# Performance work log

Measured on AMD Instinct MI355X. Metric: run time of the kernel, lower is better.

## Reference

```python
import jax, jax.numpy as jnp
import numpy as np

N_NODES = 100000
N_EDGES = 3200000
N_FEAT = 128
HIDDEN = 16
N_CLASSES = 10
N_GRAPHS = 512


def setup_inputs() -> dict:
    key = jax.random.key(0)
    ks = jax.random.split(key, 12)
    x = jax.random.normal(ks[0], (N_NODES, N_FEAT), dtype=jnp.float32)
    edge_index = jax.random.randint(ks[1], (2, N_EDGES), 0, N_NODES, dtype=jnp.int64)
    batch = jnp.sort(jax.random.randint(ks[2], (N_NODES,), 0, N_GRAPHS, dtype=jnp.int64))
    def glorot(k, fan_in, fan_out):
        s = jnp.sqrt(6.0 / (fan_in + fan_out)).astype(jnp.float32)
        return jax.random.uniform(k, (fan_in, fan_out), jnp.float32, -s, s)
    W1 = glorot(ks[3], N_FEAT, HIDDEN); b1 = jnp.zeros((HIDDEN,), jnp.float32)
    W2 = glorot(ks[4], HIDDEN, HIDDEN); b2 = jnp.zeros((HIDDEN,), jnp.float32)
    W3 = glorot(ks[5], HIDDEN, HIDDEN); b3 = jnp.zeros((HIDDEN,), jnp.float32)
    Wlin = glorot(ks[6], HIDDEN, N_CLASSES)
    blin = jnp.zeros((N_CLASSES,), jnp.float32)
    return {"x": x, "edge_index": edge_index, "batch": batch,
            "W1": W1, "b1": b1, "W2": W2, "b2": b2, "W3": W3, "b3": b3,
            "Wlin": Wlin, "blin": blin}


def _gcn_conv(x, W, b, src, dst, norm, n):
    # h = X W ; out[dst] += norm * h[src] ; + bias
    h = x @ W
    out = jax.ops.segment_sum(h[src] * norm[:, None], dst, num_segments=n)
    return out + b


def reference(x, edge_index, batch, W1, b1, W2, b2, W3, b3, Wlin, blin):
    n = x.shape[0]
    loop = jnp.arange(n, dtype=edge_index.dtype)
    src = jnp.concatenate([edge_index[0], loop])  # add self-loops (PyG GCNConv default)
    dst = jnp.concatenate([edge_index[1], loop])
    # symmetric degree normalization: deg over destination (incl. self-loops)
    deg = jax.ops.segment_sum(jnp.ones_like(dst, dtype=x.dtype), dst, num_segments=n)
    dinv = jnp.where(deg > 0, jax.lax.rsqrt(jnp.maximum(deg, 1.0)), 0.0)
    norm = dinv[src] * dinv[dst]  # [E+N]

    h = jax.nn.relu(_gcn_conv(x, W1, b1, src, dst, norm, n))
    h = jax.nn.relu(_gcn_conv(h, W2, b2, src, dst, norm, n))
    h = _gcn_conv(h, W3, b3, src, dst, norm, n)
    # global add pool over graphs
    pooled = jax.ops.segment_sum(h, batch, num_segments=N_GRAPHS)  # [G, hidden]
    # dropout p=0.5 is identity in eval mode
    return pooled @ Wlin + blin
```

## Files before the change

### kernel.cpp

```cpp
#include <hip/hip_runtime.h>
#include <hip/hip_fp16.h>

#define N_NODES   100000
#define N_EDGES   3200000
#define N_FEAT    128
#define HIDDEN    16
#define N_CLASSES 10
#define N_GRAPHS  512
#define NPB       256
#define NBUCKET   391
#define EPB       4096
#define PBLK      ((N_EDGES + EPB - 1) / EPB)
#define PSLACK    15872
#define CSLACK    11520


__global__ void init_kernel(int* __restrict__ cur, __half* __restrict__ gA, __half* __restrict__ gB) {
    int i = blockIdx.x * 256 + threadIdx.x;
    if (i < NBUCKET) cur[i] = i * PSLACK;
    if (blockIdx.x == 0) {
        int tid = threadIdx.x;
        const __half2 z2 = __floats2half2_rn(0.f, 0.f);
        if (tid < 8)       ((__half2*)(gA + (size_t)N_NODES * HIDDEN))[tid] = z2;
        else if (tid < 16) ((__half2*)(gB + (size_t)N_NODES * HIDDEN))[tid - 8] = z2;
    }
}


__global__ __launch_bounds__(512) void partition_kernel(const int* __restrict__ src,
                                                        const int* __restrict__ dst,
                                                        int* __restrict__ cur,
                                                        unsigned* __restrict__ part) {
    __shared__ int cnt[NBUCKET];
    __shared__ int lbase[NBUCKET];
    __shared__ int rk[NBUCKET];
    __shared__ int gbase[NBUCKET];
    __shared__ int s[512];
    __shared__ unsigned sorted[EPB];
    __shared__ unsigned short bb[EPB];
    __shared__ unsigned char  dl[EPB];
    int tid = threadIdx.x;
    for (int i = tid; i < NBUCKET; i += 512) cnt[i] = 0;
    __syncthreads();
    int s0 = blockIdx.x * EPB;
#pragma unroll
    for (int i = 0; i < EPB / 512; ++i) {
        int le = i * 512 + tid;
        int e  = s0 + le;
        if (e < N_EDGES) {
            int d = dst[e];
            int b = d >> 8;
            bb[le] = (unsigned short)b;
            dl[le] = (unsigned char)(d & 255);
            atomicAdd(&cnt[b], 1);
        }
    }
    __syncthreads();
    int v = (tid < NBUCKET) ? cnt[tid] : 0;
    s[tid] = v;
    __syncthreads();
    for (int off = 1; off < 512; off <<= 1) {
        int t = (tid >= off) ? s[tid - off] : 0;
        __syncthreads();
        s[tid] += t;
        __syncthreads();
    }
    if (tid < NBUCKET) {
        int lb = s[tid] - v;
        lbase[tid] = lb;
        rk[tid]    = lb;
        int cpad = (v + 15) & ~15;
        gbase[tid] = cpad ? atomicAdd(&cur[tid], cpad) : 0;
    }
    __syncthreads();
#pragma unroll
    for (int i = 0; i < EPB / 512; ++i) {
        int le = i * 512 + tid;
        int e  = s0 + le;
        if (e < N_EDGES) {
            int b = bb[le];
            int r = atomicAdd(&rk[b], 1);
            sorted[r] = (unsigned)src[e] | ((unsigned)dl[le] << 17);
        }
    }
    __syncthreads();
    int w16 = tid >> 4, l16 = tid & 15;
    for (int b = w16; b < NBUCKET; b += 32) {
        int c = cnt[b];
        if (!c) continue;
        int cpad = (c + 15) & ~15;
        int lb = lbase[b], gb = gbase[b];
        for (int j = l16; j < cpad; j += 16)
            part[gb + j] = (j < c) ? sorted[lb + j] : 0xFFFFFFFFu;
    }
}

__global__ __launch_bounds__(512) void build_csr_kernel(const unsigned* __restrict__ part,
                                                        const int* __restrict__ cur,
                                                        int2* __restrict__ rp,
                                                        float* __restrict__ dinv, int* __restrict__ csr) {
    __shared__ int ncnt[256];
    __shared__ int s[512];
    int b   = blockIdx.x;
    int tid = threadIdx.x;
    int beg = b * PSLACK, end = cur[b];
    if (tid < 256) ncnt[tid] = 0;
    __syncthreads();
    for (int j = beg + tid; j < end; j += 512) {
        unsigned r = part[j];
        if (r != 0xFFFFFFFFu) atomicAdd(&ncnt[(r >> 17) & 255], 1);
    }
    __syncthreads();
    int deg = (tid < 256) ? ncnt[tid] : 0;
    int dp  = (deg + 15) & ~15;
    s[tid] = dp;
    __syncthreads();
    for (int off = 1; off < 512; off <<= 1) {
        int t = (tid >= off) ? s[tid - off] : 0;
        __syncthreads();
        s[tid] += t;
        __syncthreads();
    }
    int excl = s[tid] - dp;
    int cbeg = b * CSLACK;
    if (tid < 256) {
        int node = b * 256 + tid;
        if (node < N_NODES) {
            rp[node]   = make_int2(cbeg + excl, cbeg + excl + dp);
            dinv[node] = rsqrtf((float)(deg + 1));
            for (int p = deg; p < dp; ++p) csr[cbeg + excl + p] = N_NODES;
        }
    }
    __syncthreads();
    if (tid < 256) ncnt[tid] = cbeg + excl;
    __syncthreads();
    for (int j = beg + tid; j < end; j += 512) {
        unsigned r = part[j];
        if (r != 0xFFFFFFFFu) {
            int vv = (r >> 17) & 255;
            int slot = atomicAdd(&ncnt[vv], 1);
            csr[slot] = (int)(r & 0x1FFFFu);
        }
    }
}


__device__ __forceinline__ void pack_store8(__half* outp, int idx, const float* o) {
    int4 w;
    __half2 q;
    q = __floats2half2_rn(o[0], o[1]); w.x = *(int*)&q;
    q = __floats2half2_rn(o[2], o[3]); w.y = *(int*)&q;
    q = __floats2half2_rn(o[4], o[5]); w.z = *(int*)&q;
    q = __floats2half2_rn(o[6], o[7]); w.w = *(int*)&q;
    ((int4*)outp)[idx] = w;
}

__global__ __launch_bounds__(256) void transform_x_kernel(const float* __restrict__ x,
                                                          const float* __restrict__ W,
                                                          const float* __restrict__ dinv,
                                                          __half* __restrict__ g) {
    __shared__ __half2 Wp[1024];
    int tid = threadIdx.x;
    for (int i = tid; i < 1024; i += 256) {
        int kp = i >> 4, f = i & 15;
        Wp[i] = __floats2half2_rn(W[(2 * kp) * HIDDEN + f], W[(2 * kp + 1) * HIDDEN + f]);
    }
    __syncthreads();
    int l  = tid & 63;
    int wv = tid >> 6;
    int rw = l >> 2;
    int q  = l & 3;
    int row = blockIdx.x * 64 + wv * 16 + rw;
    if (row >= N_NODES) return;
    const float4* xp = (const float4*)x + (size_t)row * 32;
    float4 xr[8];
#pragma unroll
    for (int s8 = 0; s8 < 8; ++s8) xr[s8] = xp[q + 4 * s8];
    __half2 acc[16];
    const __half2 z2 = __floats2half2_rn(0.f, 0.f);
#pragma unroll
    for (int f = 0; f < 16; ++f) acc[f] = z2;
    const int4* w4 = (const int4*)Wp;
#pragma unroll
    for (int s8 = 0; s8 < 8; ++s8) {
        int k4 = q + 4 * s8;
        __half2 xp0 = __floats2half2_rn(xr[s8].x, xr[s8].y);
        __half2 xp1 = __floats2half2_rn(xr[s8].z, xr[s8].w);
#pragma unroll
        for (int hf = 0; hf < 2; ++hf) {
            int kp = 2 * k4 + hf;
            __half2 xv = hf ? xp1 : xp0;
#pragma unroll
            for (int j = 0; j < 4; ++j) {
                int4 wj = w4[kp * 4 + j];
                const __half2* wvv = (const __half2*)&wj;
#pragma unroll
                for (int ff = 0; ff < 4; ++ff)
                    acc[j * 4 + ff] = __hfma2(xv, wvv[ff], acc[j * 4 + ff]);
            }
        }
    }
    float di = dinv[row];
    float o[16];
#pragma unroll
    for (int f = 0; f < 16; ++f) {
        float2 t = __half22float2(acc[f]);
        float sv = t.x + t.y;
        sv += __shfl_xor(sv, 1);
        sv += __shfl_xor(sv, 2);
        o[f] = sv * di;
    }
    if (q == 0) {
        pack_store8(g, row * 2,     &o[0]);
        pack_store8(g, row * 2 + 1, &o[8]);
    }
}

template <int MODE>
__global__ __launch_bounds__(256) void aggregate_kernel(
        const __half* __restrict__ g, const int2* __restrict__ rp,
        const int* __restrict__ csr, const float* __restrict__ dinv,
        const float* __restrict__ bias, const float* __restrict__ Wn,
        __half* __restrict__ out) {
    __shared__ float WnL[HIDDEN * HIDDEN];
    int tid  = threadIdx.x;
    int wave = tid >> 6;
    int l    = tid & 63;
    int c  = l >> 3;
    int vl = (l >> 1) & 3;
    int hh = l & 1;
    int v = blockIdx.x * 16 + wave * 4 + vl;
    int2 range = rp[v];
    if (MODE == 2) {
        if (tid < HIDDEN * HIDDEN) WnL[tid] = Wn[tid];
        __syncthreads();
    }
    int b2 = range.x >> 1;
    int K  = (range.y - range.x) >> 4;
    const int2* csr2 = (const int2*)csr;
    const int4* g4 = (const int4*)g;
    float a0 = 0.f, a1 = 0.f, a2 = 0.f, a3 = 0.f, a4 = 0.f, a5 = 0.f, a6 = 0.f, a7 = 0.f;
    for (int i = 0; i < K; ++i) {
        int2 ss = csr2[b2 + c + 8 * i];
        int4 r0 = g4[ss.x * 2 + hh];
        int4 r1 = g4[ss.y * 2 + hh];
        float2 f0 = __half22float2(*(const __half2*)&r0.x);
        float2 f1 = __half22float2(*(const __half2*)&r0.y);
        float2 f2 = __half22float2(*(const __half2*)&r0.z);
        float2 f3 = __half22float2(*(const __half2*)&r0.w);
        a0 += f0.x; a1 += f0.y; a2 += f1.x; a3 += f1.y;
        a4 += f2.x; a5 += f2.y; a6 += f3.x; a7 += f3.y;
        float2 g0 = __half22float2(*(const __half2*)&r1.x);
        float2 g1 = __half22float2(*(const __half2*)&r1.y);
        float2 g2 = __half22float2(*(const __half2*)&r1.z);
        float2 g3 = __half22float2(*(const __half2*)&r1.w);
        a0 += g0.x; a1 += g0.y; a2 += g1.x; a3 += g1.y;
        a4 += g2.x; a5 += g2.y; a6 += g3.x; a7 += g3.y;
    }
    a0 += __shfl_xor(a0, 8);  a1 += __shfl_xor(a1, 8);
    a2 += __shfl_xor(a2, 8);  a3 += __shfl_xor(a3, 8);
    a4 += __shfl_xor(a4, 8);  a5 += __shfl_xor(a5, 8);
    a6 += __shfl_xor(a6, 8);  a7 += __shfl_xor(a7, 8);
    a0 += __shfl_xor(a0, 16); a1 += __shfl_xor(a1, 16);
    a2 += __shfl_xor(a2, 16); a3 += __shfl_xor(a3, 16);
    a4 += __shfl_xor(a4, 16); a5 += __shfl_xor(a5, 16);
    a6 += __shfl_xor(a6, 16); a7 += __shfl_xor(a7, 16);
    a0 += __shfl_xor(a0, 32); a1 += __shfl_xor(a1, 32);
    a2 += __shfl_xor(a2, 32); a3 += __shfl_xor(a3, 32);
    a4 += __shfl_xor(a4, 32); a5 += __shfl_xor(a5, 32);
    a6 += __shfl_xor(a6, 32); a7 += __shfl_xor(a7, 32);
    if (c == 0) {
        int4 r = g4[v * 2 + hh];
        float2 s0 = __half22float2(*(const __half2*)&r.x);
        float2 s1 = __half22float2(*(const __half2*)&r.y);
        float2 s2 = __half22float2(*(const __half2*)&r.z);
        float2 s3 = __half22float2(*(const __half2*)&r.w);
        float di = dinv[v];
        const float4* bp = (const float4*)bias;
        float4 bA = bp[hh * 2];
        float4 bB = bp[hh * 2 + 1];
        float o[8];
        o[0] = di * (a0 + s0.x) + bA.x;
        o[1] = di * (a1 + s0.y) + bA.y;
        o[2] = di * (a2 + s1.x) + bA.z;
        o[3] = di * (a3 + s1.y) + bA.w;
        o[4] = di * (a4 + s2.x) + bB.x;
        o[5] = di * (a5 + s2.y) + bB.y;
        o[6] = di * (a6 + s3.x) + bB.z;
        o[7] = di * (a7 + s3.y) + bB.w;
        if (MODE == 2) {
#pragma unroll
            for (int i = 0; i < 8; ++i) o[i] = fmaxf(o[i], 0.f);
            float pa[16];
#pragma unroll
            for (int f = 0; f < 16; ++f) pa[f] = 0.f;
            const float* wr = &WnL[hh * 8 * HIDDEN];
#pragma unroll
            for (int qq = 0; qq < 8; ++qq) {
                float hq = o[qq];
#pragma unroll
                for (int f = 0; f < 16; ++f) pa[f] += hq * wr[qq * HIDDEN + f];
            }
            float o2[8];
#pragma unroll
            for (int i = 0; i < 8; ++i) {
                float lo = pa[i];
                float hi = pa[8 + i];
                float keep = hh ? hi : lo;
                float send = hh ? lo : hi;
                float recv = __shfl_xor(send, 1);
                o2[i] = di * (keep + recv);
            }
            pack_store8(out, v * 2 + hh, o2);
        } else {
            pack_store8(out, v * 2 + hh, o);
        }
    }
}


__global__ void pool_head_kernel(const __half* __restrict__ h, const int* __restrict__ batch,
                                 const float* __restrict__ Wlin, const float* __restrict__ blin,
                                 float* __restrict__ out) {
    __shared__ float red[256];
    __shared__ int bounds[2];
    int g   = blockIdx.x;
    int tid = threadIdx.x;
    if (tid < 2) {
        int target = g + tid;
        int lo = 0, hi = N_NODES;
        while (lo < hi) {
            int mid = (lo + hi) >> 1;
            if (batch[mid] < target) lo = mid + 1; else hi = mid;
        }
        bounds[tid] = lo;
    }
    __syncthreads();
    int start = bounds[0], end = bounds[1];
    int f = tid & 15, r = tid >> 4;
    float acc = 0.f;
    for (int v = start + r; v < end; v += 16)
        acc += __half2float(h[v * HIDDEN + f]);
    red[tid] = acc;
    __syncthreads();
    for (int off = 128; off >= 16; off >>= 1) {
        if (tid < off) red[tid] += red[tid + off];
        __syncthreads();
    }
    if (tid < N_CLASSES) {
        float s = blin[tid];
#pragma unroll
        for (int fe = 0; fe < HIDDEN; ++fe) s += red[fe] * Wlin[fe * N_CLASSES + tid];
        out[g * N_CLASSES + tid] = s;
    }
}


extern "C" void kernel_launch(void* const* d_in, const int* in_sizes, int n_in,
                              void* d_out, int out_size, void* d_ws, size_t ws_size,
                              hipStream_t stream) {
    const float* x     = (const float*)d_in[0];
    const int*   ei    = (const int*)d_in[1];
    const int*   src   = ei;
    const int*   dst   = ei + N_EDGES;
    const int*   batch = (const int*)d_in[2];
    const float* W1 = (const float*)d_in[3];
    const float* b1 = (const float*)d_in[4];
    const float* W2 = (const float*)d_in[5];
    const float* b2 = (const float*)d_in[6];
    const float* W3 = (const float*)d_in[7];
    const float* b3 = (const float*)d_in[8];
    const float* Wlin = (const float*)d_in[9];
    const float* blin = (const float*)d_in[10];
    float* out = (float*)d_out;

    char* w = (char*)d_ws;
    auto alloc = [&](size_t bytes) -> char* {
        char* p = w;
        w += (bytes + 255) & ~(size_t)255;
        return p;
    };
    int*    cur    = (int*)alloc((size_t)NBUCKET * 4);
    int2*   rp     = (int2*)alloc((size_t)N_NODES * 8);
    float*  dinv   = (float*)alloc((size_t)N_NODES * 4);
    __half* gA     = (__half*)alloc((size_t)(N_NODES + 1) * HIDDEN * 2);
    __half* gB     = (__half*)alloc((size_t)(N_NODES + 1) * HIDDEN * 2);
    __half* hA     = (__half*)alloc((size_t)(N_NODES + 1) * HIDDEN * 2);
    unsigned* part = (unsigned*)alloc((size_t)NBUCKET * PSLACK * 4);
    int*    csr    = (int*)alloc((size_t)NBUCKET * CSLACK * 4);

    int ntx = (N_NODES + 63) / 64;
    int ab  = (N_NODES + 15) / 16;

    init_kernel<<<(NBUCKET + 255) / 256, 256, 0, stream>>>(cur, gA, gB);
    partition_kernel<<<PBLK, 512, 0, stream>>>(src, dst, cur, part);
    build_csr_kernel<<<NBUCKET, 512, 0, stream>>>(part, cur, rp, dinv, csr);

    transform_x_kernel<<<ntx, 256, 0, stream>>>(x, W1, dinv, gA);
    aggregate_kernel<2><<<ab, 256, 0, stream>>>(gA, rp, csr, dinv, b1, W2, gB);
    aggregate_kernel<2><<<ab, 256, 0, stream>>>(gB, rp, csr, dinv, b2, W3, gA);
    aggregate_kernel<0><<<ab, 256, 0, stream>>>(gA, rp, csr, dinv, b3, nullptr, hA);

    pool_head_kernel<<<N_GRAPHS, 256, 0, stream>>>(hA, batch, Wlin, blin, out);
}
```

Before: 266.9 us.

## Fuse GCN pipeline into one persistent kernel with grid barriers

Replaces the seven separate launches with one persistent 512-block kernel. Phases are separated by atomic grid-wide barriers: partition, work-stolen X·W1 transform, CSR build, three aggregations and pooling. The X·W1 transform is now computed before degrees are known, written as fp32 to a temporary buffer and scaled by dinv inside the CSR build, so it can overlap with partitioning. This is meant to remove launch gaps and tail idle time, but it relies on all 512 blocks being co-resident, and the partition step now runs 256 threads per block instead of 512.

```diff
diff --git a/kernel.cpp b/kernel.cpp
--- a/kernel.cpp
+++ b/kernel.cpp
@@ -7,141 +7,39 @@
 #define HIDDEN    16
 #define N_CLASSES 10
 #define N_GRAPHS  512
-#define NPB       256
 #define NBUCKET   391
 #define EPB       4096
-#define PBLK      ((N_EDGES + EPB - 1) / EPB)
+#define PBLK      782
 #define PSLACK    15872
 #define CSLACK    11520
-
-
-__global__ void init_kernel(int* __restrict__ cur, __half* __restrict__ gA, __half* __restrict__ gB) {
-    int i = blockIdx.x * 256 + threadIdx.x;
-    if (i < NBUCKET) cur[i] = i * PSLACK;
-    if (blockIdx.x == 0) {
-        int tid = threadIdx.x;
-        const __half2 z2 = __floats2half2_rn(0.f, 0.f);
-        if (tid < 8)       ((__half2*)(gA + (size_t)N_NODES * HIDDEN))[tid] = z2;
-        else if (tid < 16) ((__half2*)(gB + (size_t)N_NODES * HIDDEN))[tid - 8] = z2;
-    }
-}
-
-
-__global__ __launch_bounds__(512) void partition_kernel(const int* __restrict__ src,
-                                                        const int* __restrict__ dst,
-                                                        int* __restrict__ cur,
-                                                        unsigned* __restrict__ part) {
-    __shared__ int cnt[NBUCKET];
-    __shared__ int lbase[NBUCKET];
-    __shared__ int rk[NBUCKET];
-    __shared__ int gbase[NBUCKET];
-    __shared__ int s[512];
-    __shared__ unsigned sorted[EPB];
-    __shared__ unsigned short bb[EPB];
-    __shared__ unsigned char  dl[EPB];
-    int tid = threadIdx.x;
-    for (int i = tid; i < NBUCKET; i += 512) cnt[i] = 0;
-    __syncthreads();
-    int s0 = blockIdx.x * EPB;
-#pragma unroll
-    for (int i = 0; i < EPB / 512; ++i) {
-        int le = i * 512 + tid;
-        int e  = s0 + le;
-        if (e < N_EDGES) {
-            int d = dst[e];
-            int b = d >> 8;
-            bb[le] = (unsigned short)b;
-            dl[le] = (unsigned char)(d & 255);
-            atomicAdd(&cnt[b], 1);
-        }
-    }
-    __syncthreads();
-    int v = (tid < NBUCKET) ? cnt[tid] : 0;
-    s[tid] = v;
-    __syncthreads();
-    for (int off = 1; off < 512; off <<= 1) {
-        int t = (tid >= off) ? s[tid - off] : 0;
-        __syncthreads();
-        s[tid] += t;
-        __syncthreads();
-    }
-    if (tid < NBUCKET) {
-        int lb = s[tid] - v;
-        lbase[tid] = lb;
-        rk[tid]    = lb;
-        int cpad = (v + 15) & ~15;
-        gbase[tid] = cpad ? atomicAdd(&cur[tid], cpad) : 0;
-    }
-    __syncthreads();
-#pragma unroll
-    for (int i = 0; i < EPB / 512; ++i) {
-        int le = i * 512 + tid;
-        int e  = s0 + le;
-        if (e < N_EDGES) {
-            int b = bb[le];
-            int r = atomicAdd(&rk[b], 1);
-            sorted[r] = (unsigned)src[e] | ((unsigned)dl[le] << 17);
-        }
-    }
-    __syncthreads();
-    int w16 = tid >> 4, l16 = tid & 15;
-    for (int b = w16; b < NBUCKET; b += 32) {
-        int c = cnt[b];
-        if (!c) continue;
-        int cpad = (c + 15) & ~15;
-        int lb = lbase[b], gb = gbase[b];
-        for (int j = l16; j < cpad; j += 16)
-            part[gb + j] = (j < c) ? sorted[lb + j] : 0xFFFFFFFFu;
-    }
-}
-
-__global__ __launch_bounds__(512) void build_csr_kernel(const unsigned* __restrict__ part,
-                                                        const int* __restrict__ cur,
-                                                        int2* __restrict__ rp,
-                                                        float* __restrict__ dinv, int* __restrict__ csr) {
-    __shared__ int ncnt[256];
-    __shared__ int s[512];
-    int b   = blockIdx.x;
-    int tid = threadIdx.x;
-    int beg = b * PSLACK, end = cur[b];
-    if (tid < 256) ncnt[tid] = 0;
-    __syncthreads();
-    for (int j = beg + tid; j < end; j += 512) {
-        unsigned r = part[j];
-        if (r != 0xFFFFFFFFu) atomicAdd(&ncnt[(r >> 17) & 255], 1);
-    }
-    __syncthreads();
-    int deg = (tid < 256) ? ncnt[tid] : 0;
-    int dp  = (deg + 15) & ~15;
-    s[tid] = dp;
-    __syncthreads();
-    for (int off = 1; off < 512; off <<= 1) {
-        int t = (tid >= off) ? s[tid - off] : 0;
-        __syncthreads();
-        s[tid] += t;
-        __syncthreads();
-    }
-    int excl = s[tid] - dp;
-    int cbeg = b * CSLACK;
-    if (tid < 256) {
-        int node = b * 256 + tid;
-        if (node < N_NODES) {
-            rp[node]   = make_int2(cbeg + excl, cbeg + excl + dp);
-            dinv[node] = rsqrtf((float)(deg + 1));
-            for (int p = deg; p < dp; ++p) csr[cbeg + excl + p] = N_NODES;
-        }
-    }
-    __syncthreads();
-    if (tid < 256) ncnt[tid] = cbeg + excl;
-    __syncthreads();
-    for (int j = beg + tid; j < end; j += 512) {
-        unsigned r = part[j];
-        if (r != 0xFFFFFFFFu) {
-            int vv = (r >> 17) & 255;
-            int slot = atomicAdd(&ncnt[vv], 1);
-            csr[slot] = (int)(r & 0x1FFFFu);
-        }
-    }
+#define GRID      512
+#define BLK       256
+#define TX_UNITS  1563
+#define AGG_UNITS 6250
+
+
+struct PartLDS {
+    int cnt[NBUCKET]; int lbase[NBUCKET]; int rk[NBUCKET]; int gbase[NBUCKET];
+    int s[512];
+    unsigned sorted[EPB];
+    unsigned short bb[EPB];
+    unsigned char  dl[EPB];
+};
+struct CsrLDS  { int ncnt[256]; int s[256]; };
+struct TxLDS   { __half2 Wp[1024]; };
+struct AggLDS  { float WnL[256]; };
+struct PoolLDS { float red[256]; int bounds[2]; };
+union AllLDS { PartLDS p; CsrLDS c; TxLDS t; AggLDS a; PoolLDS o; };
+
+
+__device__ __forceinline__ void grid_sync(int* bar, int target) {
+    __syncthreads();
+    if (threadIdx.x == 0) {
+        __hip_atomic_fetch_add(bar, 1, __ATOMIC_ACQ_REL, __HIP_MEMORY_SCOPE_AGENT);
+        while (__hip_atomic_load(bar, __ATOMIC_ACQUIRE, __HIP_MEMORY_SCOPE_AGENT) < target)
+            __builtin_amdgcn_s_sleep(2);
+    }
+    __syncthreads();
 }
 
 
@@ -155,22 +53,131 @@
     ((int4*)outp)[idx] = w;
 }
 
-__global__ __launch_bounds__(256) void transform_x_kernel(const float* __restrict__ x,
-                                                          const float* __restrict__ W,
-                                                          const float* __restrict__ dinv,
-                                                          __half* __restrict__ g) {
-    __shared__ __half2 Wp[1024];
+
+__device__ void partition_block(int pb, const int* __restrict__ src, const int* __restrict__ dst,
+                                int* __restrict__ cur, unsigned* __restrict__ part, PartLDS& L) {
     int tid = threadIdx.x;
-    for (int i = tid; i < 1024; i += 256) {
-        int kp = i >> 4, f = i & 15;
-        Wp[i] = __floats2half2_rn(W[(2 * kp) * HIDDEN + f], W[(2 * kp + 1) * HIDDEN + f]);
-    }
-    __syncthreads();
+    for (int i = tid; i < NBUCKET; i += BLK) L.cnt[i] = 0;
+    __syncthreads();
+    int s0 = pb * EPB;
+#pragma unroll
+    for (int i = 0; i < EPB / BLK; ++i) {
+        int le = i * BLK + tid;
+        int e  = s0 + le;
+        if (e < N_EDGES) {
+            int d = dst[e];
+            int b = d >> 8;
+            L.bb[le] = (unsigned short)b;
+            L.dl[le] = (unsigned char)(d & 255);
+            atomicAdd(&L.cnt[b], 1);
+        }
+    }
+    __syncthreads();
+    int t2 = tid + 256;
+    int v0 = (tid < NBUCKET) ? L.cnt[tid] : 0;
+    int v1 = (t2  < NBUCKET) ? L.cnt[t2]  : 0;
+    L.s[tid] = v0; L.s[t2] = v1;
+    __syncthreads();
+    for (int off = 1; off < 512; off <<= 1) {
+        int a = (tid >= off) ? L.s[tid - off] : 0;
+        int b = (t2  >= off) ? L.s[t2  - off] : 0;
+        __syncthreads();
+        L.s[tid] += a; L.s[t2] += b;
+        __syncthreads();
+    }
+    if (tid < NBUCKET) {
+        int lb = L.s[tid] - v0;
+        L.lbase[tid] = lb; L.rk[tid] = lb;
+        int cpad = (v0 + 15) & ~15;
+        L.gbase[tid] = cpad ? atomicAdd(&cur[tid], cpad) : 0;
+    }
+    if (t2 < NBUCKET) {
+        int lb = L.s[t2] - v1;
+        L.lbase[t2] = lb; L.rk[t2] = lb;
+        int cpad = (v1 + 15) & ~15;
+        L.gbase[t2] = cpad ? atomicAdd(&cur[t2], cpad) : 0;
+    }
+    __syncthreads();
+#pragma unroll
+    for (int i = 0; i < EPB / BLK; ++i) {
+        int le = i * BLK + tid;
+        int e  = s0 + le;
+        if (e < N_EDGES) {
+            int b = L.bb[le];
+            int r = atomicAdd(&L.rk[b], 1);
+            L.sorted[r] = (unsigned)src[e] | ((unsigned)L.dl[le] << 17);
+        }
+    }
+    __syncthreads();
+    int w16 = tid >> 4, l16 = tid & 15;
+    for (int b = w16; b < NBUCKET; b += 16) {
+        int c = L.cnt[b];
+        if (!c) continue;
+        int cpad = (c + 15) & ~15;
+        int lb = L.lbase[b], gb = L.gbase[b];
+        for (int j = l16; j < cpad; j += 16)
+            part[gb + j] = (j < c) ? L.sorted[lb + j] : 0xFFFFFFFFu;
+    }
+}
+
+__device__ void csr_block(int b, const unsigned* __restrict__ part, const int* __restrict__ cur,
+                          int2* __restrict__ rp, float* __restrict__ dinv, int* __restrict__ csr,
+                          const float* __restrict__ xw, __half* __restrict__ gA, CsrLDS& L) {
+    int tid = threadIdx.x;
+    int beg = b * PSLACK, end = cur[b];
+    L.ncnt[tid] = 0;
+    __syncthreads();
+    for (int j = beg + tid; j < end; j += BLK) {
+        unsigned r = part[j];
+        if (r != 0xFFFFFFFFu) atomicAdd(&L.ncnt[(r >> 17) & 255], 1);
+    }
+    __syncthreads();
+    int deg = L.ncnt[tid];
+    int dp  = (deg + 15) & ~15;
+    L.s[tid] = dp;
+    __syncthreads();
+    for (int off = 1; off < 256; off <<= 1) {
+        int t = (tid >= off) ? L.s[tid - off] : 0;
+        __syncthreads();
+        L.s[tid] += t;
+        __syncthreads();
+    }
+    int excl = L.s[tid] - dp;
+    int cbeg = b * CSLACK;
+    int node = b * 256 + tid;
+    if (node < N_NODES) {
+        rp[node] = make_int2(cbeg + excl, cbeg + excl + dp);
+        float di = rsqrtf((float)(deg + 1));
+        dinv[node] = di;
+        for (int p = deg; p < dp; ++p) csr[cbeg + excl + p] = N_NODES;
+        const float4* ip = (const float4*)(xw + (size_t)node * 16);
+        float4 v0 = ip[0], v1 = ip[1], v2 = ip[2], v3 = ip[3];
+        float o0[8] = {v0.x*di, v0.y*di, v0.z*di, v0.w*di, v1.x*di, v1.y*di, v1.z*di, v1.w*di};
+        float o1[8] = {v2.x*di, v2.y*di, v2.z*di, v2.w*di, v3.x*di, v3.y*di, v3.z*di, v3.w*di};
+        pack_store8(gA, node * 2,     o0);
+        pack_store8(gA, node * 2 + 1, o1);
+    }
+    __syncthreads();
+    L.ncnt[tid] = cbeg + excl;
+    __syncthreads();
+    for (int j = beg + tid; j < end; j += BLK) {
+        unsigned r = part[j];
+        if (r != 0xFFFFFFFFu) {
+            int vv = (r >> 17) & 255;
+            int slot = atomicAdd(&L.ncnt[vv], 1);
+            csr[slot] = (int)(r & 0x1FFFFu);
+        }
+    }
+}
+
+__device__ __forceinline__ void tx_unit(int u, const float* __restrict__ x,
+                                        float* __restrict__ xw, const __half2* Wp) {
+    int tid = threadIdx.x;
     int l  = tid & 63;
     int wv = tid >> 6;
     int rw = l >> 2;
     int q  = l & 3;
-    int row = blockIdx.x * 64 + wv * 16 + rw;
+    int row = u * 64 + wv * 16 + rw;
     if (row >= N_NODES) return;
     const float4* xp = (const float4*)x + (size_t)row * 32;
     float4 xr[8];
@@ -200,7 +207,6 @@
             }
         }
     }
-    float di = dinv[row];
     float o[16];
 #pragma unroll
     for (int f = 0; f < 16; ++f) {
@@ -208,151 +214,214 @@
         float sv = t.x + t.y;
         sv += __shfl_xor(sv, 1);
         sv += __shfl_xor(sv, 2);
-        o[f] = sv * di;
+        o[f] = sv;
     }
     if (q == 0) {
-        pack_store8(g, row * 2,     &o[0]);
-        pack_store8(g, row * 2 + 1, &o[8]);
+        float4* op = (float4*)(xw + (size_t)row * 16);
+        op[0] = make_float4(o[0],  o[1],  o[2],  o[3]);
+        op[1] = make_float4(o[4],  o[5],  o[6],  o[7]);
+        op[2] = make_float4(o[8],  o[9],  o[10], o[11]);
+        op[3] = make_float4(o[12], o[13], o[14], o[15]);
     }
 }
 
 template <int MODE>
-__global__ __launch_bounds__(256) void aggregate_kernel(
-        const __half* __restrict__ g, const int2* __restrict__ rp,
-        const int* __restrict__ csr, const float* __restrict__ dinv,
-        const float* __restrict__ bias, const float* __restrict__ Wn,
-        __half* __restrict__ out) {
-    __shared__ float WnL[HIDDEN * HIDDEN];
-    int tid  = threadIdx.x;
+__device__ void agg_phase(const __half* __restrict__ g, const int2* __restrict__ rp,
+                          const int* __restrict__ csr, const float* __restrict__ dinv,
+                          const float* __restrict__ bias, const float* __restrict__ Wn,
+                          __half* __restrict__ out, AggLDS& L) {
+    int tid = threadIdx.x;
+    if (MODE == 2) L.WnL[tid] = Wn[tid];
+    __syncthreads();
     int wave = tid >> 6;
     int l    = tid & 63;
     int c  = l >> 3;
     int vl = (l >> 1) & 3;
     int hh = l & 1;
-    int v = blockIdx.x * 16 + wave * 4 + vl;
-    int2 range = rp[v];
-    if (MODE == 2) {
-        if (tid < HIDDEN * HIDDEN) WnL[tid] = Wn[tid];
-        __syncthreads();
-    }
-    int b2 = range.x >> 1;
-    int K  = (range.y - range.x) >> 4;
     const int2* csr2 = (const int2*)csr;
     const int4* g4 = (const int4*)g;
-    float a0 = 0.f, a1 = 0.f, a2 = 0.f, a3 = 0.f, a4 = 0.f, a5 = 0.f, a6 = 0.f, a7 = 0.f;
-    for (int i = 0; i < K; ++i) {
-        int2 ss = csr2[b2 + c + 8 * i];
-        int4 r0 = g4[ss.x * 2 + hh];
-        int4 r1 = g4[ss.y * 2 + hh];
-        float2 f0 = __half22float2(*(const __half2*)&r0.x);
-        float2 f1 = __half22float2(*(const __half2*)&r0.y);
-        float2 f2 = __half22float2(*(const __half2*)&r0.z);
-        float2 f3 = __half22float2(*(const __half2*)&r0.w);
-        a0 += f0.x; a1 += f0.y; a2 += f1.x; a3 += f1.y;
-        a4 += f2.x; a5 += f2.y; a6 += f3.x; a7 += f3.y;
-        float2 g0 = __half22float2(*(const __half2*)&r1.x);
-        float2 g1 = __half22float2(*(const __half2*)&r1.y);
-        float2 g2 = __half22float2(*(const __half2*)&r1.z);
-        float2 g3 = __half22float2(*(const __half2*)&r1.w);
-        a0 += g0.x; a1 += g0.y; a2 += g1.x; a3 += g1.y;
-        a4 += g2.x; a5 += g2.y; a6 += g3.x; a7 += g3.y;
-    }
-    a0 += __shfl_xor(a0, 8);  a1 += __shfl_xor(a1, 8);
-    a2 += __shfl_xor(a2, 8);  a3 += __shfl_xor(a3, 8);
-    a4 += __shfl_xor(a4, 8);  a5 += __shfl_xor(a5, 8);
-    a6 += __shfl_xor(a6, 8);  a7 += __shfl_xor(a7, 8);
-    a0 += __shfl_xor(a0, 16); a1 += __shfl_xor(a1, 16);
-    a2 += __shfl_xor(a2, 16); a3 += __shfl_xor(a3, 16);
-    a4 += __shfl_xor(a4, 16); a5 += __shfl_xor(a5, 16);
-    a6 += __shfl_xor(a6, 16); a7 += __shfl_xor(a7, 16);
-    a0 += __shfl_xor(a0, 32); a1 += __shfl_xor(a1, 32);
-    a2 += __shfl_xor(a2, 32); a3 += __shfl_xor(a3, 32);
-    a4 += __shfl_xor(a4, 32); a5 += __shfl_xor(a5, 32);
-    a6 += __shfl_xor(a6, 32); a7 += __shfl_xor(a7, 32);
-    if (c == 0) {
-        int4 r = g4[v * 2 + hh];
-        float2 s0 = __half22float2(*(const __half2*)&r.x);
-        float2 s1 = __half22float2(*(const __half2*)&r.y);
-        float2 s2 = __half22float2(*(const __half2*)&r.z);
-        float2 s3 = __half22float2(*(const __half2*)&r.w);
-        float di = dinv[v];
-        const float4* bp = (const float4*)bias;
-        float4 bA = bp[hh * 2];
-        float4 bB = bp[hh * 2 + 1];
-        float o[8];
-        o[0] = di * (a0 + s0.x) + bA.x;
-        o[1] = di * (a1 + s0.y) + bA.y;
-        o[2] = di * (a2 + s1.x) + bA.z;
-        o[3] = di * (a3 + s1.y) + bA.w;
-        o[4] = di * (a4 + s2.x) + bB.x;
-        o[5] = di * (a5 + s2.y) + bB.y;
-        o[6] = di * (a6 + s3.x) + bB.z;
-        o[7] = di * (a7 + s3.y) + bB.w;
-        if (MODE == 2) {
-#pragma unroll
-            for (int i = 0; i < 8; ++i) o[i] = fmaxf(o[i], 0.f);
-            float pa[16];
-#pragma unroll
-            for (int f = 0; f < 16; ++f) pa[f] = 0.f;
-            const float* wr = &WnL[hh * 8 * HIDDEN];
-#pragma unroll
-            for (int qq = 0; qq < 8; ++qq) {
-                float hq = o[qq];
-#pragma unroll
-                for (int f = 0; f < 16; ++f) pa[f] += hq * wr[qq * HIDDEN + f];
+    for (int unit = blockIdx.x; unit < AGG_UNITS; unit += GRID) {
+        int v = unit * 16 + wave * 4 + vl;
+        int2 range = rp[v];
+        int b2 = range.x >> 1;
+        int K  = (range.y - range.x) >> 4;
+        float a0 = 0.f, a1 = 0.f, a2 = 0.f, a3 = 0.f, a4 = 0.f, a5 = 0.f, a6 = 0.f, a7 = 0.f;
+        for (int i = 0; i < K; ++i) {
+            int2 ss = csr2[b2 + c + 8 * i];
+            int4 r0 = g4[ss.x * 2 + hh];
+            int4 r1 = g4[ss.y * 2 + hh];
+            float2 f0 = __half22float2(*(const __half2*)&r0.x);
+            float2 f1 = __half22float2(*(const __half2*)&r0.y);
+            float2 f2 = __half22float2(*(const __half2*)&r0.z);
+            float2 f3 = __half22float2(*(const __half2*)&r0.w);
+            a0 += f0.x; a1 += f0.y; a2 += f1.x; a3 += f1.y;
+            a4 += f2.x; a5 += f2.y; a6 += f3.x; a7 += f3.y;
+            float2 g0 = __half22float2(*(const __half2*)&r1.x);
+            float2 g1 = __half22float2(*(const __half2*)&r1.y);
+            float2 g2 = __half22float2(*(const __half2*)&r1.z);
+            float2 g3 = __half22float2(*(const __half2*)&r1.w);
+            a0 += g0.x; a1 += g0.y; a2 += g1.x; a3 += g1.y;
+            a4 += g2.x; a5 += g2.y; a6 += g3.x; a7 += g3.y;
+        }
+        a0 += __shfl_xor(a0, 8);  a1 += __shfl_xor(a1, 8);
+        a2 += __shfl_xor(a2, 8);  a3 += __shfl_xor(a3, 8);
+        a4 += __shfl_xor(a4, 8);  a5 += __shfl_xor(a5, 8);
+        a6 += __shfl_xor(a6, 8);  a7 += __shfl_xor(a7, 8);
+        a0 += __shfl_xor(a0, 16); a1 += __shfl_xor(a1, 16);
+        a2 += __shfl_xor(a2, 16); a3 += __shfl_xor(a3, 16);
+        a4 += __shfl_xor(a4, 16); a5 += __shfl_xor(a5, 16);
+        a6 += __shfl_xor(a6, 16); a7 += __shfl_xor(a7, 16);
+        a0 += __shfl_xor(a0, 32); a1 += __shfl_xor(a1, 32);
+        a2 += __shfl_xor(a2, 32); a3 += __shfl_xor(a3, 32);
+        a4 += __shfl_xor(a4, 32); a5 += __shfl_xor(a5, 32);
+        a6 += __shfl_xor(a6, 32); a7 += __shfl_xor(a7, 32);
+        if (c == 0) {
+            int4 r = g4[v * 2 + hh];
+            float2 s0 = __half22float2(*(const __half2*)&r.x);
+            float2 s1 = __half22float2(*(const __half2*)&r.y);
+            float2 s2 = __half22float2(*(const __half2*)&r.z);
+            float2 s3 = __half22float2(*(const __half2*)&r.w);
+            float di = dinv[v];
+            const float4* bp = (const float4*)bias;
+            float4 bA = bp[hh * 2];
+            float4 bB = bp[hh * 2 + 1];
+            float o[8];
+            o[0] = di * (a0 + s0.x) + bA.x;
+            o[1] = di * (a1 + s0.y) + bA.y;
+            o[2] = di * (a2 + s1.x) + bA.z;
+            o[3] = di * (a3 + s1.y) + bA.w;
+            o[4] = di * (a4 + s2.x) + bB.x;
+            o[5] = di * (a5 + s2.y) + bB.y;
+            o[6] = di * (a6 + s3.x) + bB.z;
+            o[7] = di * (a7 + s3.y) + bB.w;
+            if (MODE == 2) {
+#pragma unroll
+                for (int i = 0; i < 8; ++i) o[i] = fmaxf(o[i], 0.f);
+                float pa[16];
+#pragma unroll
+                for (int f = 0; f < 16; ++f) pa[f] = 0.f;
+                const float* wr = &L.WnL[hh * 8 * HIDDEN];
+#pragma unroll
+                for (int qq = 0; qq < 8; ++qq) {
+                    float hq = o[qq];
+#pragma unroll
+                    for (int f = 0; f < 16; ++f) pa[f] += hq * wr[qq * HIDDEN + f];
+                }
+                float o2[8];
+#pragma unroll
+                for (int i = 0; i < 8; ++i) {
+                    float lo = pa[i];
+                    float hi = pa[8 + i];
+                    float keep = hh ? hi : lo;
+                    float send = hh ? lo : hi;
+                    float recv = __shfl_xor(send, 1);
+                    o2[i] = di * (keep + recv);
+                }
+                pack_store8(out, v * 2 + hh, o2);
+            } else {
+                pack_store8(out, v * 2 + hh, o);
             }
-            float o2[8];
-#pragma unroll
-            for (int i = 0; i < 8; ++i) {
-                float lo = pa[i];
-                float hi = pa[8 + i];
-                float keep = hh ? hi : lo;
-                float send = hh ? lo : hi;
-                float recv = __shfl_xor(send, 1);
-                o2[i] = di * (keep + recv);
-            }
-            pack_store8(out, v * 2 + hh, o2);
-        } else {
-            pack_store8(out, v * 2 + hh, o);
-        }
-    }
-}
-
-
-__global__ void pool_head_kernel(const __half* __restrict__ h, const int* __restrict__ batch,
-                                 const float* __restrict__ Wlin, const float* __restrict__ blin,
-                                 float* __restrict__ out) {
-    __shared__ float red[256];
-    __shared__ int bounds[2];
-    int g   = blockIdx.x;
+        }
+    }
+}
+
+__device__ void pool_block(int gph, const __half* __restrict__ h, const int* __restrict__ batch,
+                           const float* __restrict__ Wlin, const float* __restrict__ blin,
+                           float* __restrict__ out, PoolLDS& L) {
     int tid = threadIdx.x;
     if (tid < 2) {
-        int target = g + tid;
+        int target = gph + tid;
         int lo = 0, hi = N_NODES;
         while (lo < hi) {
             int mid = (lo + hi) >> 1;
             if (batch[mid] < target) lo = mid + 1; else hi = mid;
         }
-        bounds[tid] = lo;
-    }
-    __syncthreads();
-    int start = bounds[0], end = bounds[1];
+        L.bounds[tid] = lo;
+    }
+    __syncthreads();
+    int start = L.bounds[0], end = L.bounds[1];
     int f = tid & 15, r = tid >> 4;
     float acc = 0.f;
     for (int v = start + r; v < end; v += 16)
         acc += __half2float(h[v * HIDDEN + f]);
-    red[tid] = acc;
+    L.red[tid] = acc;
     __syncthreads();
     for (int off = 128; off >= 16; off >>= 1) {
-        if (tid < off) red[tid] += red[tid + off];
+        if (tid < off) L.red[tid] += L.red[tid + off];
         __syncthreads();
     }
     if (tid < N_CLASSES) {
         float s = blin[tid];
 #pragma unroll
-        for (int fe = 0; fe < HIDDEN; ++fe) s += red[fe] * Wlin[fe * N_CLASSES + tid];
-        out[g * N_CLASSES + tid] = s;
-    }
+        for (int fe = 0; fe < HIDDEN; ++fe) s += L.red[fe] * Wlin[fe * N_CLASSES + tid];
+        out[gph * N_CLASSES + tid] = s;
+    }
+    __syncthreads();
+}
+
+
+__global__ void init_kernel(int* __restrict__ cur, int* __restrict__ txc, int* __restrict__ bar,
+                            __half* __restrict__ gA, __half* __restrict__ gB) {
+    int i = blockIdx.x * 256 + threadIdx.x;
+    if (i < NBUCKET) cur[i] = i * PSLACK;
+    if (i == NBUCKET)     *txc = 0;
+    if (i == NBUCKET + 1) *bar = 0;
+    if (blockIdx.x == 0) {
+        const __half2 z2 = __floats2half2_rn(0.f, 0.f);
+        int tid = threadIdx.x;
+        if (tid < 8)       ((__half2*)(gA + (size_t)N_NODES * HIDDEN))[tid] = z2;
+        else if (tid < 16) ((__half2*)(gB + (size_t)N_NODES * HIDDEN))[tid - 8] = z2;
+    }
+}
+
+
+__global__ __launch_bounds__(BLK, 4) void mega_kernel(
+        const float* __restrict__ x, const int* __restrict__ src, const int* __restrict__ dst,
+        const int* __restrict__ batch,
+        const float* __restrict__ W1, const float* __restrict__ b1,
+        const float* __restrict__ W2, const float* __restrict__ b2,
+        const float* __restrict__ W3, const float* __restrict__ b3,
+        const float* __restrict__ Wlin, const float* __restrict__ blin,
+        float* __restrict__ out,
+        int* __restrict__ cur, int2* __restrict__ rp, float* __restrict__ dinv,
+        float* __restrict__ xw, __half* __restrict__ gA, __half* __restrict__ gB,
+        __half* __restrict__ hA, unsigned* __restrict__ part, int* __restrict__ csr,
+        int* __restrict__ txc, int* __restrict__ bar) {
+    __shared__ AllLDS lds;
+    __shared__ int steal_u;
+    int bid = blockIdx.x, tid = threadIdx.x;
+
+    for (int pb = bid; pb < PBLK; pb += GRID) {
+        partition_block(pb, src, dst, cur, part, lds.p);
+        __syncthreads();
+    }
+    for (int i = tid; i < 1024; i += BLK) {
+        int kp = i >> 4, f = i & 15;
+        lds.t.Wp[i] = __floats2half2_rn(W1[(2 * kp) * HIDDEN + f], W1[(2 * kp + 1) * HIDDEN + f]);
+    }
+    __syncthreads();
+    while (true) {
+        if (tid == 0) steal_u = atomicAdd(txc, 1);
+        __syncthreads();
+        int u = steal_u;
+        __syncthreads();
+        if (u >= TX_UNITS) break;
+        tx_unit(u, x, xw, lds.t.Wp);
+    }
+    grid_sync(bar, 1 * GRID);
+
+    if (bid < NBUCKET)
+        csr_block(bid, part, cur, rp, dinv, csr, xw, gA, lds.c);
+    grid_sync(bar, 2 * GRID);
+
+    agg_phase<2>(gA, rp, csr, dinv, b1, W2, gB, lds.a);
+    grid_sync(bar, 3 * GRID);
+    agg_phase<2>(gB, rp, csr, dinv, b2, W3, gA, lds.a);
+    grid_sync(bar, 4 * GRID);
+    agg_phase<0>(gA, rp, csr, dinv, b3, nullptr, hA, lds.a);
+    grid_sync(bar, 5 * GRID);
+
+    pool_block(bid, hA, batch, Wlin, blin, out, lds.o);
 }
 
 
@@ -380,26 +449,21 @@
         w += (bytes + 255) & ~(size_t)255;
         return p;
     };
-    int*    cur    = (int*)alloc((size_t)NBUCKET * 4);
-    int2*   rp     = (int2*)alloc((size_t)N_NODES * 8);
-    float*  dinv   = (float*)alloc((size_t)N_NODES * 4);
-    __half* gA     = (__half*)alloc((size_t)(N_NODES + 1) * HIDDEN * 2);
-    __half* gB     = (__half*)alloc((size_t)(N_NODES + 1) * HIDDEN * 2);
-    __half* hA     = (__half*)alloc((size_t)(N_NODES + 1) * HIDDEN * 2);
+    int*    cur  = (int*)alloc((size_t)NBUCKET * 4);
+    int*    txc  = (int*)alloc(256);
+    int*    bar  = (int*)alloc(256);
+    int2*   rp   = (int2*)alloc((size_t)N_NODES * 8);
+    float*  dinv = (float*)alloc((size_t)N_NODES * 4);
+    float*  xw   = (float*)alloc((size_t)N_NODES * HIDDEN * 4);
+    __half* gA   = (__half*)alloc((size_t)(N_NODES + 1) * HIDDEN * 2);
+    __half* gB   = (__half*)alloc((size_t)(N_NODES + 1) * HIDDEN * 2);
+    __half* hA   = (__half*)alloc((size_t)(N_NODES + 1) * HIDDEN * 2);
     unsigned* part = (unsigned*)alloc((size_t)NBUCKET * PSLACK * 4);
-    int*    csr    = (int*)alloc((size_t)NBUCKET * CSLACK * 4);
-
-    int ntx = (N_NODES + 63) / 64;
-    int ab  = (N_NODES + 15) / 16;
-
-    init_kernel<<<(NBUCKET + 255) / 256, 256, 0, stream>>>(cur, gA, gB);
-    partition_kernel<<<PBLK, 512, 0, stream>>>(src, dst, cur, part);
-    build_csr_kernel<<<NBUCKET, 512, 0, stream>>>(part, cur, rp, dinv, csr);
-
-    transform_x_kernel<<<ntx, 256, 0, stream>>>(x, W1, dinv, gA);
-    aggregate_kernel<2><<<ab, 256, 0, stream>>>(gA, rp, csr, dinv, b1, W2, gB);
-    aggregate_kernel<2><<<ab, 256, 0, stream>>>(gB, rp, csr, dinv, b2, W3, gA);
-    aggregate_kernel<0><<<ab, 256, 0, stream>>>(gA, rp, csr, dinv, b3, nullptr, hA);
-
-    pool_head_kernel<<<N_GRAPHS, 256, 0, stream>>>(hA, batch, Wlin, blin, out);
-}
+    int*    csr  = (int*)alloc((size_t)NBUCKET * CSLACK * 4);
+
+    init_kernel<<<2, 256, 0, stream>>>(cur, txc, bar, gA, gB);
+    mega_kernel<<<GRID, BLK, 0, stream>>>(x, src, dst, batch,
+                                          W1, b1, W2, b2, W3, b3, Wlin, blin, out,
+                                          cur, rp, dinv, xw, gA, gB, hA, part, csr,
+                                          txc, bar);
+}
```

Result: slower. 851.6 us (+219.0%).
